# Kernel optimization log

Measured on AMD Instinct MI355X. Metric: run time of the kernel, lower is better.

The kernel has to match this reference:

```python
import math
import jax, jax.numpy as jnp
import numpy as np

EPS = 1e-12
NHEAD = 12
HEAD_DIM = 64  # d_model // nhead = 768 // 12


def setup_inputs() -> dict:
    key = jax.random.key(0)
    ks = jax.random.split(key, 8)
    L, D, H = 12, 768, 2048
    B, S = 8, 1024
    std = 0.02
    return {
        "x": jax.random.normal(ks[0], (B, S, D), jnp.float32),
        "wq": jax.random.normal(ks[1], (L, D, D), jnp.float32) * std,
        "wk": jax.random.normal(ks[2], (L, D, D), jnp.float32) * std,
        "wv": jax.random.normal(ks[3], (L, D, D), jnp.float32) * std,
        "wo": jax.random.normal(ks[4], (L, D, D), jnp.float32) * std,
        "w1": jax.random.normal(ks[5], (L, H, D), jnp.float32) * std,
        "w2": jax.random.normal(ks[6], (L, D, H), jnp.float32) * std,
        "attn_norm_w": jnp.ones((L, D), jnp.float32),
        "ffn_norm_w": jnp.ones((L, D), jnp.float32),
    }


def _rmsnorm(x, w):
    # x * rsqrt(mean(x^2) + eps) * w
    return x * jax.lax.rsqrt(jnp.mean(x * x, axis=-1, keepdims=True) + EPS) * w


def _block(x, params):
    wq, wk, wv, wo, w1, w2, anw, fnw = params
    B, S, D = x.shape
    # --- attention (manual matmul-softmax-matmul, fp32 softmax) ---
    xn = _rmsnorm(x, anw)
    q = jnp.einsum('bsd,ed->bse', xn, wq).reshape(B, S, NHEAD, HEAD_DIM)
    k = jnp.einsum('bsd,ed->bse', xn, wk).reshape(B, S, NHEAD, HEAD_DIM)
    v = jnp.einsum('bsd,ed->bse', xn, wv).reshape(B, S, NHEAD, HEAD_DIM)
    scores = jnp.einsum('bqhd,bkhd->bhqk', q, k) / math.sqrt(HEAD_DIM)
    probs = jax.nn.softmax(scores.astype(jnp.float32), axis=-1).astype(x.dtype)
    attn = jnp.einsum('bhqk,bkhd->bqhd', probs, v).reshape(B, S, D)
    h = x + jnp.einsum('bsd,ed->bse', attn, wo)
    # --- FFN: w2(silu(w1(h_norm))) ---
    hn = _rmsnorm(h, fnw)
    ff = jnp.einsum('bsh,dh->bsd', jax.nn.silu(jnp.einsum('bsd,hd->bsh', hn, w1)), w2)
    return h + ff


def reference(x, wq, wk, wv, wo, w1, w2, attn_norm_w, ffn_norm_w):
    def step(carry, p):
        return _block(carry, p), None
    out, _ = jax.lax.scan(step, x, (wq, wk, wv, wo, w1, w2, attn_norm_w, ffn_norm_w))
    return out
```

## Files before the change

### kernel.cpp

```cpp
#include <hip/hip_runtime.h>
#include <stdint.h>

typedef unsigned short u16;
typedef unsigned int u32;
typedef __bf16 bf16x8 __attribute__((ext_vector_type(8)));
typedef __bf16 bf16x4 __attribute__((ext_vector_type(4)));
typedef float f32x4 __attribute__((ext_vector_type(4)));

__device__ __forceinline__ u16 f2bf(float f) {
  u32 u = __builtin_bit_cast(u32, f);
  u32 r = (u + 0x7FFFu + ((u >> 16) & 1u)) >> 16;
  return (u16)r;
}

__global__ __launch_bounds__(256)
void convert_w(const float* __restrict__ wq, const float* __restrict__ wk,
               const float* __restrict__ wv, const float* __restrict__ wo,
               const float* __restrict__ w1, const float* __restrict__ w2,
               u16* __restrict__ out) {
  size_t i = ((size_t)blockIdx.x * 256 + threadIdx.x) * 4;
  if (i >= 5505024) return;
  const float* src; size_t off;
  if (i < 589824)       { src = wq; off = i; }
  else if (i < 1179648) { src = wk; off = i - 589824; }
  else if (i < 1769472) { src = wv; off = i - 1179648; }
  else if (i < 2359296) { src = wo; off = i - 1769472; }
  else if (i < 3932160) { src = w1; off = i - 2359296; }
  else                  { src = w2; off = i - 3932160; }
  float4 v = *(const float4*)(src + off);
  u32 lo = (u32)f2bf(v.x) | ((u32)f2bf(v.y) << 16);
  u32 hi = (u32)f2bf(v.z) | ((u32)f2bf(v.w) << 16);
  *(uint2*)(out + i) = make_uint2(lo, hi);
}

__device__ __forceinline__ void rn_store4(u16* p, float4 v, float4 w, float sc) {
  u32 lo = (u32)f2bf(v.x * sc * w.x) | ((u32)f2bf(v.y * sc * w.y) << 16);
  u32 hi = (u32)f2bf(v.z * sc * w.z) | ((u32)f2bf(v.w * sc * w.w) << 16);
  *(uint2*)p = make_uint2(lo, hi);
}

__global__ __launch_bounds__(256)
void rmsnorm_k(const float* __restrict__ x, const float* __restrict__ w,
               u16* __restrict__ out) {
  const int tok = (blockIdx.x << 2) + (threadIdx.x >> 6);
  const int l = threadIdx.x & 63;
  const float* xr = x + (size_t)tok * 768;
  float4 v0 = *(const float4*)(xr + l * 4);
  float4 v1 = *(const float4*)(xr + 256 + l * 4);
  float4 v2 = *(const float4*)(xr + 512 + l * 4);
  float ss = v0.x*v0.x + v0.y*v0.y + v0.z*v0.z + v0.w*v0.w
           + v1.x*v1.x + v1.y*v1.y + v1.z*v1.z + v1.w*v1.w
           + v2.x*v2.x + v2.y*v2.y + v2.z*v2.z + v2.w*v2.w;
  ss += __shfl_xor(ss, 1);  ss += __shfl_xor(ss, 2);  ss += __shfl_xor(ss, 4);
  ss += __shfl_xor(ss, 8);  ss += __shfl_xor(ss, 16); ss += __shfl_xor(ss, 32);
  float sc = rsqrtf(ss * (1.f / 768.f) + 1e-12f);
  float4 w0 = *(const float4*)(w + l * 4);
  float4 w1v = *(const float4*)(w + 256 + l * 4);
  float4 w2v = *(const float4*)(w + 512 + l * 4);
  u16* o = out + (size_t)tok * 768;
  rn_store4(o + l * 4, v0, w0, sc);
  rn_store4(o + 256 + l * 4, v1, w1v, sc);
  rn_store4(o + 512 + l * 4, v2, w2v, sc);
}

#define GEMM_CORE(A_, W_, K_, m0_, n0_)                                             \
  for (int kt = 0; kt < (K_); kt += 64) {                                           \
    __syncthreads();                                                                \
    _Pragma("unroll")                                                               \
    for (int ii = 0; ii < 4; ++ii) {                                                \
      int issue = (w << 2) + ii;                                                    \
      int r = (issue << 3) + (l >> 3);                                              \
      int c = (l & 7) ^ (r & 7);                                                    \
      __builtin_amdgcn_global_load_lds((A_) + (size_t)((m0_) + r) * (K_) + kt + c * 8, \
                                       As + issue * 512, 16, 0, 0);                 \
      __builtin_amdgcn_global_load_lds((W_) + (size_t)((n0_) + r) * (K_) + kt + c * 8, \
                                       Ws + issue * 512, 16, 0, 0);                 \
    }                                                                               \
    __syncthreads();                                                                \
    _Pragma("unroll")                                                               \
    for (int kc = 0; kc < 2; ++kc) {                                                \
      int chunk = lg + (kc << 2);                                                   \
      bf16x8 af[4], bfr[4];                                                         \
      _Pragma("unroll")                                                             \
      for (int i = 0; i < 4; ++i) {                                                 \
        int mr = (wm << 6) + (i << 4) + ll;                                         \
        af[i] = *(const bf16x8*)((const char*)As + mr * 128 + ((chunk ^ (mr & 7)) << 4)); \
        int nr = (wn << 6) + (i << 4) + ll;                                         \
        bfr[i] = *(const bf16x8*)((const char*)Ws + nr * 128 + ((chunk ^ (nr & 7)) << 4)); \
      }                                                                             \
      _Pragma("unroll")                                                             \
      for (int i = 0; i < 4; ++i)                                                   \
        _Pragma("unroll")                                                           \
        for (int j = 0; j < 4; ++j)                                                 \
          acc[i][j] = __builtin_amdgcn_mfma_f32_16x16x32_bf16(af[i], bfr[j], acc[i][j], 0, 0, 0); \
    }                                                                               \
  }

template<int EP>
__global__ __launch_bounds__(256, 2)
void gemm_bt(const u16* __restrict__ A, const u16* __restrict__ W,
             void* __restrict__ outp, const float* __restrict__ Res,
             int M, int N, int K) {
  __shared__ __align__(16) u16 As[128 * 64];
  __shared__ __align__(16) u16 Ws[128 * 64];
  const int tid = threadIdx.x;
  const int w = tid >> 6, l = tid & 63;
  const int lg = l >> 4, ll = l & 15;
  const int ntiles = N >> 7;
  const int mt = blockIdx.x / ntiles, nt = blockIdx.x - mt * ntiles;
  const int m0 = mt << 7, n0 = nt << 7;
  const int wm = w >> 1, wn = w & 1;

  const f32x4 fz = {0.f, 0.f, 0.f, 0.f};
  f32x4 acc[4][4];
#pragma unroll
  for (int i = 0; i < 4; ++i)
#pragma unroll
    for (int j = 0; j < 4; ++j) acc[i][j] = fz;

  GEMM_CORE(A, W, K, m0, n0)

  const int g4 = lg << 2;
#pragma unroll
  for (int i = 0; i < 4; ++i) {
#pragma unroll
    for (int j = 0; j < 4; ++j) {
      int row0 = m0 + (wm << 6) + (i << 4) + g4;
      int col = n0 + (wn << 6) + (j << 4) + ll;
      f32x4 v = acc[i][j];
      if (EP == 0) {
        u16* o = (u16*)outp;
#pragma unroll
        for (int e = 0; e < 4; ++e) o[(size_t)(row0 + e) * N + col] = f2bf(v[e]);
      } else if (EP == 1) {
        float* o = (float*)outp;
#pragma unroll
        for (int e = 0; e < 4; ++e) {
          size_t idx = (size_t)(row0 + e) * N + col;
          o[idx] = Res[idx] + v[e];
        }
      } else {
        u16* o = (u16*)outp;
#pragma unroll
        for (int e = 0; e < 4; ++e) {
          float xx = v[e];
          o[(size_t)(row0 + e) * N + col] = f2bf(xx / (1.f + __expf(-xx)));
        }
      }
    }
  }
}

__global__ __launch_bounds__(256, 4)
void gemm_bt64(const u16* __restrict__ A, const u16* __restrict__ W,
               float* __restrict__ outp, const float* __restrict__ Res,
               int M, int N, int K) {
  __shared__ __align__(16) u16 As[64 * 64];
  __shared__ __align__(16) u16 Ws[128 * 64];
  const int tid = threadIdx.x;
  const int w = tid >> 6, l = tid & 63;
  const int lg = l >> 4, ll = l & 15;
  const int ntiles = N >> 7;
  const int mt = blockIdx.x / ntiles, nt = blockIdx.x - mt * ntiles;
  const int m0 = mt << 6, n0 = nt << 7;
  const int wm = w >> 1, wn = w & 1;

  const f32x4 fz = {0.f, 0.f, 0.f, 0.f};
  f32x4 acc[2][4];
#pragma unroll
  for (int i = 0; i < 2; ++i)
#pragma unroll
    for (int j = 0; j < 4; ++j) acc[i][j] = fz;

  for (int kt = 0; kt < K; kt += 64) {
    __syncthreads();
#pragma unroll
    for (int ii = 0; ii < 6; ++ii) {
      int issue = w * 6 + ii;
      if (issue < 8) {
        int r = (issue << 3) + (l >> 3);
        int c = (l & 7) ^ (r & 7);
        __builtin_amdgcn_global_load_lds(A + (size_t)(m0 + r) * K + kt + c * 8,
                                         As + issue * 512, 16, 0, 0);
      } else {
        int is2 = issue - 8;
        int r = (is2 << 3) + (l >> 3);
        int c = (l & 7) ^ (r & 7);
        __builtin_amdgcn_global_load_lds(W + (size_t)(n0 + r) * K + kt + c * 8,
                                         Ws + is2 * 512, 16, 0, 0);
      }
    }
    __syncthreads();
#pragma unroll
    for (int kc = 0; kc < 2; ++kc) {
      int chunk = lg + (kc << 2);
      bf16x8 af[2], bfr[4];
#pragma unroll
      for (int i = 0; i < 2; ++i) {
        int mr = (wm << 5) + (i << 4) + ll;
        af[i] = *(const bf16x8*)((const char*)As + mr * 128 + ((chunk ^ (mr & 7)) << 4));
      }
#pragma unroll
      for (int j = 0; j < 4; ++j) {
        int nr = (wn << 6) + (j << 4) + ll;
        bfr[j] = *(const bf16x8*)((const char*)Ws + nr * 128 + ((chunk ^ (nr & 7)) << 4));
      }
#pragma unroll
      for (int i = 0; i < 2; ++i)
#pragma unroll
        for (int j = 0; j < 4; ++j)
          acc[i][j] = __builtin_amdgcn_mfma_f32_16x16x32_bf16(af[i], bfr[j], acc[i][j], 0, 0, 0);
    }
  }

  const int g4 = lg << 2;
#pragma unroll
  for (int i = 0; i < 2; ++i) {
#pragma unroll
    for (int j = 0; j < 4; ++j) {
      int row0 = m0 + (wm << 5) + (i << 4) + g4;
      int col = n0 + (wn << 6) + (j << 4) + ll;
      f32x4 v = acc[i][j];
#pragma unroll
      for (int e = 0; e < 4; ++e) {
        size_t idx = (size_t)(row0 + e) * N + col;
        outp[idx] = Res[idx] + v[e];
      }
    }
  }
}

__global__ __launch_bounds__(256, 2)
void gemm_qkv(const u16* __restrict__ A, const u16* __restrict__ W,
              u16* __restrict__ Qo, u16* __restrict__ Ko, u16* __restrict__ Vo) {
  __shared__ __align__(16) u16 As[128 * 64];
  __shared__ __align__(16) u16 Ws[128 * 64];
  const int tid = threadIdx.x;
  const int w = tid >> 6, l = tid & 63;
  const int lg = l >> 4, ll = l & 15;
  const int mt = blockIdx.x / 18, nt = blockIdx.x - mt * 18;
  const int m0 = mt << 7, n0 = nt << 7;
  const int wm = w >> 1, wn = w & 1;
  const int K = 768;

  const f32x4 fz = {0.f, 0.f, 0.f, 0.f};
  f32x4 acc[4][4];
#pragma unroll
  for (int i = 0; i < 4; ++i)
#pragma unroll
    for (int j = 0; j < 4; ++j) acc[i][j] = fz;

  GEMM_CORE(A, W, K, m0, n0)

  const int g4 = lg << 2;
#pragma unroll
  for (int i = 0; i < 4; ++i) {
#pragma unroll
    for (int j = 0; j < 4; ++j) {
      int row0 = m0 + (wm << 6) + (i << 4) + g4;
      int col = n0 + (wn << 6) + (j << 4) + ll;
      f32x4 v = acc[i][j];
      if (nt < 12) {
        u16* o = (nt < 6) ? Qo : Ko;
        int c = (nt < 6) ? col : (col - 768);
#pragma unroll
        for (int e = 0; e < 4; ++e) o[(size_t)(row0 + e) * 768 + c] = f2bf(v[e]);
      } else {
        int c = col - 1536;
        int vrow = ((row0 >> 10) * 768) + c;
        u32 lo = (u32)f2bf(v[0]) | ((u32)f2bf(v[1]) << 16);
        u32 hi = (u32)f2bf(v[2]) | ((u32)f2bf(v[3]) << 16);
        *(uint2*)(Vo + ((size_t)vrow << 10) + (row0 & 1023)) = make_uint2(lo, hi);
      }
    }
  }
}

__global__ __launch_bounds__(256, 2)
void attn_kernel(const u16* __restrict__ Q, const u16* __restrict__ Kg,
                 const u16* __restrict__ Vt, u16* __restrict__ Og) {
  __shared__ __align__(16) __bf16 Ks[128 * 64];
  __shared__ __align__(16) __bf16 Vs[64 * 128];

  const int tid = threadIdx.x;
  const int w = tid >> 6, l = tid & 63;
  const int lg = l >> 4, ll = l & 15;
  const int bid = blockIdx.x;
  const int qt = bid / 96;
  const int bh = bid - qt * 96;
  const int b = bh / 12, hh = bh - b * 12;
  const float SC = 0.125f * 1.44269504f;

  __bf16* Pw = Ks + (w << 11);

  bf16x8 qf[2];
  const int tq0 = (b << 10) + (qt << 6) + (w << 4);
#pragma unroll
  for (int kc = 0; kc < 2; ++kc)
    qf[kc] = *(const bf16x8*)(Q + (size_t)(tq0 + ll) * 768 + hh * 64 + kc * 32 + lg * 8);

  bf16x8 kp[4], vp[4];
#define ISSUE_KV(t_)                                                                  \
  { _Pragma("unroll")                                                                 \
    for (int ii = 0; ii < 4; ++ii) {                                                  \
      int issue = (w << 2) + ii;                                                      \
      int r = (issue << 3) + (l >> 3);                                                \
      int c = (l & 7) ^ (r & 7);                                                      \
      kp[ii] = *(const bf16x8*)(Kg + (size_t)((b << 10) + ((t_) << 7) + r) * 768 + hh * 64 + c * 8); \
      int rv = (issue << 2) + (l >> 4);                                               \
      int cv = ll ^ (rv & 7);                                                         \
      vp[ii] = *(const bf16x8*)(Vt + (size_t)((bh << 6) + rv) * 1024 + ((t_) << 7) + cv * 8); \
    } }
#define WRITE_KV                                                                      \
  { _Pragma("unroll")                                                                 \
    for (int ii = 0; ii < 4; ++ii) {                                                  \
      int issue = (w << 2) + ii;                                                      \
      *(bf16x8*)((char*)Ks + issue * 1024 + l * 16) = kp[ii];                         \
      *(bf16x8*)((char*)Vs + issue * 1024 + l * 16) = vp[ii];                         \
    } }

  const f32x4 fz = {0.f, 0.f, 0.f, 0.f};
  f32x4 oacc[4];
#pragma unroll
  for (int i = 0; i < 4; ++i) oacc[i] = fz;
  float mrow = -1e30f, lrow = 0.f;

  ISSUE_KV(0);
  WRITE_KV;
  __syncthreads();

  for (int kt = 0; kt < 8; ++kt) {
    if (kt < 7) ISSUE_KV(kt + 1);

    f32x4 sa[8];
#pragma unroll
    for (int fn = 0; fn < 8; ++fn) sa[fn] = fz;
    __builtin_amdgcn_s_setprio(1);
#pragma unroll
    for (int kc = 0; kc < 2; ++kc) {
      int chunk = lg + (kc << 2);
      bf16x8 kb[8];
#pragma unroll
      for (int fn = 0; fn < 8; ++fn) {
        int nr = (fn << 4) + ll;
        kb[fn] = *(const bf16x8*)((const char*)Ks + nr * 128 + ((chunk ^ (nr & 7)) << 4));
      }
#pragma unroll
      for (int fn = 0; fn < 8; ++fn)
        sa[fn] = __builtin_amdgcn_mfma_f32_16x16x32_bf16(kb[fn], qf[kc], sa[fn], 0, 0, 0);
    }
    __builtin_amdgcn_s_setprio(0);

    __syncthreads();

    f32x4 vm = sa[0];
#pragma unroll
    for (int fn = 1; fn < 8; ++fn) {
#pragma unroll
      for (int e = 0; e < 4; ++e) vm[e] = fmaxf(vm[e], sa[fn][e]);
    }
    float mx = fmaxf(fmaxf(vm[0], vm[1]), fmaxf(vm[2], vm[3]));
    mx = fmaxf(mx, __shfl_xor(mx, 16));
    mx = fmaxf(mx, __shfl_xor(mx, 32));
    float mnew = fmaxf(mrow, mx);
    float c2 = mnew * SC;
    float scal = __builtin_amdgcn_exp2f(__builtin_fmaf(SC, mrow, -c2));

    f32x4 vsum = fz;
#pragma unroll
    for (int fn = 0; fn < 8; ++fn) {
      f32x4 p;
#pragma unroll
      for (int e = 0; e < 4; ++e)
        p[e] = __builtin_amdgcn_exp2f(__builtin_fmaf(SC, sa[fn][e], -c2));
      vsum += p;
      bf16x4 pv4;
#pragma unroll
      for (int e = 0; e < 4; ++e) pv4[e] = (__bf16)p[e];
      int chunk = (fn << 1) + (lg >> 1);
      *(bf16x4*)((char*)Pw + ll * 256 + ((chunk ^ (ll & 7)) << 4) + ((lg & 1) << 3)) = pv4;
    }
    float rs = (vsum[0] + vsum[1]) + (vsum[2] + vsum[3]);
    rs += __shfl_xor(rs, 16);
    rs += __shfl_xor(rs, 32);
    lrow = lrow * scal + rs;
    mrow = mnew;

    asm volatile("" ::: "memory");

#pragma unroll
    for (int fd = 0; fd < 4; ++fd) oacc[fd] *= scal;

    __builtin_amdgcn_s_setprio(1);
#pragma unroll
    for (int ch = 0; ch < 4; ++ch) {
      int chunk = lg + (ch << 2);
      bf16x8 pb = *(const bf16x8*)((const char*)Pw + ll * 256 + ((chunk ^ (ll & 7)) << 4));
#pragma unroll
      for (int fd = 0; fd < 4; ++fd) {
        int dr = (fd << 4) + ll;
        bf16x8 av = *(const bf16x8*)((const char*)Vs + dr * 256 + ((chunk ^ (dr & 7)) << 4));
        oacc[fd] = __builtin_amdgcn_mfma_f32_16x16x32_bf16(av, pb, oacc[fd], 0, 0, 0);
      }
    }
    __builtin_amdgcn_s_setprio(0);

    asm volatile("" ::: "memory");

    if (kt < 7) {
      __syncthreads();
      WRITE_KV;
      __syncthreads();
    }
  }
#undef ISSUE_KV
#undef WRITE_KV

  float inv = 1.f / lrow;
#pragma unroll
  for (int fd = 0; fd < 4; ++fd) {
    f32x4 v = oacc[fd];
    int d0 = (fd << 4) + (lg << 2);
    u16* o = Og + (size_t)(tq0 + ll) * 768 + hh * 64 + d0;
    u32 lo = (u32)f2bf(v[0] * inv) | ((u32)f2bf(v[1] * inv) << 16);
    u32 hi = (u32)f2bf(v[2] * inv) | ((u32)f2bf(v[3] * inv) << 16);
    *(uint2*)o = make_uint2(lo, hi);
  }
}

extern "C" void kernel_launch(void* const* d_in, const int* in_sizes, int n_in,
                              void* d_out, int out_size, void* d_ws, size_t ws_size,
                              hipStream_t stream) {
  const float* x = (const float*)d_in[0];
  const float* wq = (const float*)d_in[1];
  const float* wk = (const float*)d_in[2];
  const float* wv = (const float*)d_in[3];
  const float* wo = (const float*)d_in[4];
  const float* w1 = (const float*)d_in[5];
  const float* w2 = (const float*)d_in[6];
  const float* anw = (const float*)d_in[7];
  const float* fnw = (const float*)d_in[8];

  char* ws = (char*)d_ws;
  float* h    = (float*)(ws);
  u16* xn     = (u16*)(ws + 25165824);
  u16* qb     = (u16*)(ws + 37748736);
  u16* kb     = (u16*)(ws + 50331648);
  u16* vt     = (u16*)(ws + 62914560);
  u16* ff1    = (u16*)(ws + 75497472);
  u16* wbuf   = (u16*)(ws + 109051904);

  hipMemcpyAsync(h, x, 25165824, hipMemcpyDeviceToDevice, stream);

  for (int L = 0; L < 12; ++L) {
    convert_w<<<5376, 256, 0, stream>>>(
        wq + (size_t)L * 589824, wk + (size_t)L * 589824,
        wv + (size_t)L * 589824, wo + (size_t)L * 589824,
        w1 + (size_t)L * 1572864, w2 + (size_t)L * 1572864, wbuf);
    rmsnorm_k<<<2048, 256, 0, stream>>>(h, anw + L * 768, xn);
    gemm_qkv<<<1152, 256, 0, stream>>>(xn, wbuf, qb, kb, vt);
    attn_kernel<<<1536, 256, 0, stream>>>(qb, kb, vt, qb);
    gemm_bt64<<<768, 256, 0, stream>>>(qb, wbuf + 1769472, h, h, 8192, 768, 768);
    rmsnorm_k<<<2048, 256, 0, stream>>>(h, fnw + L * 768, xn);
    gemm_bt<2><<<1024, 256, 0, stream>>>(xn, wbuf + 2359296, ff1, nullptr, 8192, 2048, 768);
    float* outw = (L == 11) ? (float*)d_out : h;
    gemm_bt64<<<768, 256, 0, stream>>>(ff1, wbuf + 3932160, outw, h, 8192, 768, 2048);
  }
}
```

Measured before the change: 2.647 ms.

## Replace FFN up-projection GEMM with 256x256 8-wave pipelined direct-to-LDS kernel

Replaces the 128x128 FFN1+SiLU GEMM with a 512-thread kernel that computes 256x256 tiles. It stages data through eight LDS buffers using global_load_lds and overlaps loads with MFMA phases, using explicit vmcnt waits and s_barrier. The attention kernel's __syncthreads are also swapped for a lighter lgkmcnt wait plus s_barrier. The aim is more data reuse per tile and fewer pipeline stalls, at the cost of only 256 blocks and fragile hand-written synchronization.

```diff
diff --git a/kernel.cpp b/kernel.cpp
--- a/kernel.cpp
+++ b/kernel.cpp
@@ -96,61 +96,6 @@
     }                                                                               \
   }
 
-template<int EP>
-__global__ __launch_bounds__(256, 2)
-void gemm_bt(const u16* __restrict__ A, const u16* __restrict__ W,
-             void* __restrict__ outp, const float* __restrict__ Res,
-             int M, int N, int K) {
-  __shared__ __align__(16) u16 As[128 * 64];
-  __shared__ __align__(16) u16 Ws[128 * 64];
-  const int tid = threadIdx.x;
-  const int w = tid >> 6, l = tid & 63;
-  const int lg = l >> 4, ll = l & 15;
-  const int ntiles = N >> 7;
-  const int mt = blockIdx.x / ntiles, nt = blockIdx.x - mt * ntiles;
-  const int m0 = mt << 7, n0 = nt << 7;
-  const int wm = w >> 1, wn = w & 1;
-
-  const f32x4 fz = {0.f, 0.f, 0.f, 0.f};
-  f32x4 acc[4][4];
-#pragma unroll
-  for (int i = 0; i < 4; ++i)
-#pragma unroll
-    for (int j = 0; j < 4; ++j) acc[i][j] = fz;
-
-  GEMM_CORE(A, W, K, m0, n0)
-
-  const int g4 = lg << 2;
-#pragma unroll
-  for (int i = 0; i < 4; ++i) {
-#pragma unroll
-    for (int j = 0; j < 4; ++j) {
-      int row0 = m0 + (wm << 6) + (i << 4) + g4;
-      int col = n0 + (wn << 6) + (j << 4) + ll;
-      f32x4 v = acc[i][j];
-      if (EP == 0) {
-        u16* o = (u16*)outp;
-#pragma unroll
-        for (int e = 0; e < 4; ++e) o[(size_t)(row0 + e) * N + col] = f2bf(v[e]);
-      } else if (EP == 1) {
-        float* o = (float*)outp;
-#pragma unroll
-        for (int e = 0; e < 4; ++e) {
-          size_t idx = (size_t)(row0 + e) * N + col;
-          o[idx] = Res[idx] + v[e];
-        }
-      } else {
-        u16* o = (u16*)outp;
-#pragma unroll
-        for (int e = 0; e < 4; ++e) {
-          float xx = v[e];
-          o[(size_t)(row0 + e) * N + col] = f2bf(xx / (1.f + __expf(-xx)));
-        }
-      }
-    }
-  }
-}
-
 __global__ __launch_bounds__(256, 4)
 void gemm_bt64(const u16* __restrict__ A, const u16* __restrict__ W,
                float* __restrict__ outp, const float* __restrict__ Res,
@@ -276,6 +221,194 @@
   }
 }
 
+#define G8_BARSYNC  __builtin_amdgcn_s_barrier(); \
+                    asm volatile("s_waitcnt lgkmcnt(0)" ::: "memory")
+#define G8_END      __builtin_amdgcn_s_barrier()
+#define G8_VMW4     asm volatile("s_waitcnt vmcnt(4)" ::: "memory")
+
+__global__ __launch_bounds__(512, 2)
+void gemm8p_silu(const u16* __restrict__ A, const u16* __restrict__ W,
+                 u16* __restrict__ out) {
+  __shared__ __align__(16) u16 LB[8][8192];
+  const int tid = threadIdx.x;
+  const int w = tid >> 6, l = tid & 63;
+  const int lg = l >> 4, ll = l & 15;
+  const int wm = w >> 2, wn = w & 3;
+  const int mt = blockIdx.x >> 3, nt = blockIdx.x & 7;
+  const int m0 = mt << 8, n0 = nt << 8;
+  const int K = 768;
+
+  const f32x4 fz = {0.f, 0.f, 0.f, 0.f};
+  f32x4 acc[8][4];
+#pragma unroll
+  for (int i = 0; i < 8; ++i)
+#pragma unroll
+    for (int j = 0; j < 4; ++j) acc[i][j] = fz;
+
+#define STG8(Mat, base0, tile_, half_, s_)                                          \
+  { _Pragma("unroll")                                                               \
+    for (int ii = 0; ii < 2; ++ii) {                                                \
+      int r = ii * 64 + w * 8 + (l >> 3);                                           \
+      int cg = (l & 7) ^ (r & 7);                                                   \
+      __builtin_amdgcn_global_load_lds(                                             \
+          (Mat) + (size_t)((base0) + (half_) * 128 + r) * 768 + (tile_) * 64 + cg * 8, \
+          &LB[s_][(ii * 64 + w * 8) * 64], 16, 0, 0);                               \
+    } }
+
+  auto LDA = [&](int par, int mf, int kc) -> bf16x8 {
+    int rr = (mf & 3) * 32 + wm * 16 + ll;
+    return *(const bf16x8*)((const char*)&LB[(par << 1) + (mf >> 2)][0]
+                            + rr * 128 + ((((kc << 2) + lg) ^ (rr & 7)) << 4));
+  };
+  auto LDB = [&](int par, int nf, int kc) -> bf16x8 {
+    int cc = (nf & 1) * 64 + wn * 16 + ll;
+    return *(const bf16x8*)((const char*)&LB[4 + (par << 1) + (nf >> 1)][0]
+                            + cc * 128 + ((((kc << 2) + lg) ^ (cc & 7)) << 4));
+  };
+
+  STG8(A, m0, 0, 0, 0); STG8(W, n0, 0, 0, 4);
+  STG8(A, m0, 0, 1, 1); STG8(W, n0, 0, 1, 5);
+  STG8(A, m0, 1, 0, 2); STG8(W, n0, 1, 0, 6);
+  G8_VMW4;
+  __builtin_amdgcn_s_barrier();
+
+  bf16x8 a[4][2], b[4][2];
+
+#define G8_MFMA(MFBASE, NFBASE)                                                     \
+  __builtin_amdgcn_s_setprio(1);                                                    \
+  _Pragma("unroll")                                                                 \
+  for (int mi = 0; mi < 4; ++mi)                                                    \
+    _Pragma("unroll")                                                               \
+    for (int nj = 0; nj < 2; ++nj)                                                  \
+      _Pragma("unroll")                                                             \
+      for (int kc = 0; kc < 2; ++kc)                                                \
+        acc[(MFBASE) + mi][(NFBASE) + nj] = __builtin_amdgcn_mfma_f32_16x16x32_bf16( \
+            a[mi][kc], b[(NFBASE) + nj][kc], acc[(MFBASE) + mi][(NFBASE) + nj], 0, 0, 0); \
+  __builtin_amdgcn_s_setprio(0)
+
+  for (int t = 0; t < 10; t += 2) {
+#pragma unroll
+    for (int mi = 0; mi < 4; ++mi)
+#pragma unroll
+      for (int kc = 0; kc < 2; ++kc) a[mi][kc] = LDA(0, mi, kc);
+#pragma unroll
+    for (int nj = 0; nj < 2; ++nj)
+#pragma unroll
+      for (int kc = 0; kc < 2; ++kc) b[nj][kc] = LDB(0, nj, kc);
+    STG8(A, m0, t + 1, 1, 3);
+    G8_BARSYNC; G8_MFMA(0, 0); G8_END;
+#pragma unroll
+    for (int nj = 2; nj < 4; ++nj)
+#pragma unroll
+      for (int kc = 0; kc < 2; ++kc) b[nj][kc] = LDB(0, nj, kc);
+    STG8(W, n0, t + 1, 1, 7);
+    G8_BARSYNC; G8_MFMA(0, 2); G8_END;
+#pragma unroll
+    for (int mi = 0; mi < 4; ++mi)
+#pragma unroll
+      for (int kc = 0; kc < 2; ++kc) a[mi][kc] = LDA(0, 4 + mi, kc);
+    STG8(A, m0, t + 2, 0, 0);
+    G8_BARSYNC; G8_MFMA(4, 0); G8_END;
+    STG8(W, n0, t + 2, 0, 4);
+    G8_VMW4;
+    __builtin_amdgcn_s_barrier();
+    G8_MFMA(4, 2); G8_END;
+#pragma unroll
+    for (int mi = 0; mi < 4; ++mi)
+#pragma unroll
+      for (int kc = 0; kc < 2; ++kc) a[mi][kc] = LDA(1, mi, kc);
+#pragma unroll
+    for (int nj = 0; nj < 2; ++nj)
+#pragma unroll
+      for (int kc = 0; kc < 2; ++kc) b[nj][kc] = LDB(1, nj, kc);
+    STG8(A, m0, t + 2, 1, 1);
+    STG8(W, n0, t + 2, 1, 5);
+    G8_BARSYNC; G8_MFMA(0, 0); G8_END;
+#pragma unroll
+    for (int nj = 2; nj < 4; ++nj)
+#pragma unroll
+      for (int kc = 0; kc < 2; ++kc) b[nj][kc] = LDB(1, nj, kc);
+    G8_BARSYNC; G8_MFMA(0, 2); G8_END;
+#pragma unroll
+    for (int mi = 0; mi < 4; ++mi)
+#pragma unroll
+      for (int kc = 0; kc < 2; ++kc) a[mi][kc] = LDA(1, 4 + mi, kc);
+    STG8(A, m0, t + 3, 0, 2);
+    G8_BARSYNC; G8_MFMA(4, 0); G8_END;
+    STG8(W, n0, t + 3, 0, 6);
+    G8_VMW4;
+    __builtin_amdgcn_s_barrier();
+    G8_MFMA(4, 2); G8_END;
+  }
+
+  {
+#pragma unroll
+    for (int mi = 0; mi < 4; ++mi)
+#pragma unroll
+      for (int kc = 0; kc < 2; ++kc) a[mi][kc] = LDA(0, mi, kc);
+#pragma unroll
+    for (int nj = 0; nj < 2; ++nj)
+#pragma unroll
+      for (int kc = 0; kc < 2; ++kc) b[nj][kc] = LDB(0, nj, kc);
+    STG8(A, m0, 11, 1, 3);
+    G8_BARSYNC; G8_MFMA(0, 0); G8_END;
+#pragma unroll
+    for (int nj = 2; nj < 4; ++nj)
+#pragma unroll
+      for (int kc = 0; kc < 2; ++kc) b[nj][kc] = LDB(0, nj, kc);
+    STG8(W, n0, 11, 1, 7);
+    G8_BARSYNC; G8_MFMA(0, 2); G8_END;
+#pragma unroll
+    for (int mi = 0; mi < 4; ++mi)
+#pragma unroll
+      for (int kc = 0; kc < 2; ++kc) a[mi][kc] = LDA(0, 4 + mi, kc);
+    G8_BARSYNC; G8_MFMA(4, 0); G8_END;
+    asm volatile("s_waitcnt vmcnt(0)" ::: "memory");
+    __builtin_amdgcn_s_barrier();
+    G8_MFMA(4, 2); G8_END;
+#pragma unroll
+    for (int mi = 0; mi < 4; ++mi)
+#pragma unroll
+      for (int kc = 0; kc < 2; ++kc) a[mi][kc] = LDA(1, mi, kc);
+#pragma unroll
+    for (int nj = 0; nj < 2; ++nj)
+#pragma unroll
+      for (int kc = 0; kc < 2; ++kc) b[nj][kc] = LDB(1, nj, kc);
+    G8_BARSYNC; G8_MFMA(0, 0); G8_END;
+#pragma unroll
+    for (int nj = 2; nj < 4; ++nj)
+#pragma unroll
+      for (int kc = 0; kc < 2; ++kc) b[nj][kc] = LDB(1, nj, kc);
+    G8_BARSYNC; G8_MFMA(0, 2); G8_END;
+#pragma unroll
+    for (int mi = 0; mi < 4; ++mi)
+#pragma unroll
+      for (int kc = 0; kc < 2; ++kc) a[mi][kc] = LDA(1, 4 + mi, kc);
+    G8_BARSYNC; G8_MFMA(4, 0); G8_END;
+    G8_BARSYNC; G8_MFMA(4, 2); G8_END;
+  }
+#undef STG8
+#undef G8_MFMA
+
+#pragma unroll
+  for (int mf = 0; mf < 8; ++mf) {
+#pragma unroll
+    for (int nf = 0; nf < 4; ++nf) {
+      int row0 = m0 + mf * 32 + wm * 16 + (lg << 2);
+      int col = n0 + nf * 64 + wn * 16 + ll;
+      f32x4 v = acc[mf][nf];
+#pragma unroll
+      for (int e = 0; e < 4; ++e) {
+        float xx = v[e];
+        out[(size_t)(row0 + e) * 2048 + col] = f2bf(xx / (1.f + __expf(-xx)));
+      }
+    }
+  }
+}
+
+#define AT_SYNC  asm volatile("s_waitcnt lgkmcnt(0)" ::: "memory"); \
+                 __builtin_amdgcn_s_barrier();                      \
+                 asm volatile("" ::: "memory")
 __global__ __launch_bounds__(256, 2)
 void attn_kernel(const u16* __restrict__ Q, const u16* __restrict__ Kg,
                  const u16* __restrict__ Vt, u16* __restrict__ Og) {
@@ -327,7 +460,7 @@
 
   ISSUE_KV(0);
   WRITE_KV;
-  __syncthreads();
+  AT_SYNC;
 
   for (int kt = 0; kt < 8; ++kt) {
     if (kt < 7) ISSUE_KV(kt + 1);
@@ -351,7 +484,7 @@
     }
     __builtin_amdgcn_s_setprio(0);
 
-    __syncthreads();
+    AT_SYNC;
 
     f32x4 vm = sa[0];
 #pragma unroll
@@ -405,12 +538,10 @@
     }
     __builtin_amdgcn_s_setprio(0);
 
-    asm volatile("" ::: "memory");
-
     if (kt < 7) {
-      __syncthreads();
+      AT_SYNC;
       WRITE_KV;
-      __syncthreads();
+      AT_SYNC;
     }
   }
 #undef ISSUE_KV
@@ -462,7 +593,7 @@
     attn_kernel<<<1536, 256, 0, stream>>>(qb, kb, vt, qb);
     gemm_bt64<<<768, 256, 0, stream>>>(qb, wbuf + 1769472, h, h, 8192, 768, 768);
     rmsnorm_k<<<2048, 256, 0, stream>>>(h, fnw + L * 768, xn);
-    gemm_bt<2><<<1024, 256, 0, stream>>>(xn, wbuf + 2359296, ff1, nullptr, 8192, 2048, 768);
+    gemm8p_silu<<<256, 512, 0, stream>>>(xn, wbuf + 2359296, ff1);
     float* outw = (L == 11) ? (float*)d_out : h;
     gemm_bt64<<<768, 256, 0, stream>>>(ff1, wbuf + 3932160, outw, h, 8192, 768, 2048);
   }
```

Result: no change. 2.662 ms (+0.6%).
